# Optimization experiments

Measured on AMD Instinct MI355X. Metric: run time of the kernel, lower is better.

## Reference

```python
import jax, jax.numpy as jnp
from jax import lax
import numpy as np

B, S, D, H, DO, E, K = 4, 2048, 1024, 4096, 1024, 8, 2
CAP_FACTOR = 1.5
LN_EPS = 1e-5


def setup_inputs() -> dict:
    key = jax.random.key(0)
    ks = jax.random.split(key, 8)
    s_in = 1.0 / np.sqrt(D)
    s_h = 1.0 / np.sqrt(H)
    return {
        "x": jax.random.normal(ks[0], (B, S, D), dtype=jnp.float32),
        "router_w": jax.random.normal(ks[1], (D, E), dtype=jnp.float32) * s_in,
        "router_b": jnp.zeros((E,), dtype=jnp.float32),
        "w1": jax.random.normal(ks[2], (E, D, H), dtype=jnp.float32) * s_in,
        "b1": jnp.zeros((E, H), dtype=jnp.float32),
        "w2": jax.random.normal(ks[3], (E, H, DO), dtype=jnp.float32) * s_h,
        "b2": jnp.zeros((E, DO), dtype=jnp.float32),
        "ln_g": jnp.ones((DO,), dtype=jnp.float32),
        "ln_b": jnp.zeros((DO,), dtype=jnp.float32),
    }


def reference(x, router_w, router_b, w1, b1, w2, b2, ln_g, ln_b):
    # Eval-mode (dropout = identity), faithful to SparseDispatcher.forward.
    Bx, Sx, Dx = x.shape
    N = Bx * Sx                               # total tokens
    capacity = max(int(N * CAP_FACTOR / E), K)

    logits = jnp.einsum("bsd,de->bse", x, router_w) + router_b
    probs = jax.nn.softmax(logits, axis=-1)   # [B,S,E]
    topv, topi = lax.top_k(probs, K)          # [B,S,K]
    topv = topv / topv.sum(axis=-1, keepdims=True)

    flat_i = topi.reshape(-1)                 # [N*K] expert ids
    flat_v = topv.reshape(-1)                 # [N*K] combine weights

    # Per-expert capacity selection: keep top-`capacity` assignments by prob.
    mask = flat_i[None, :] == jnp.arange(E)[:, None]          # [E, N*K]
    prio = jnp.where(mask, flat_v[None, :], -1.0)             # [E, N*K]
    pv, pp = lax.top_k(prio, capacity)                        # [E, cap]
    valid = pv > 0.0
    tok = jnp.where(valid, pp // K, 0)                        # token index per slot
    w = jnp.where(valid, pv, 0.0)                             # combine weight (0 if padded)

    x_flat = x.reshape(N, Dx)
    xin = x_flat[tok]                                         # [E, cap, D] gather
    h = jax.nn.gelu(jnp.einsum("ecd,edh->ech", xin, w1) + b1[:, None, :],
                    approximate=False)
    out_e = jnp.einsum("ech,eho->eco", h, w2) + b2[:, None, :]  # [E, cap, DO]
    out_e = out_e * w[..., None]

    out = jnp.zeros((N, DO), dtype=x.dtype)
    out = out.at[tok.reshape(-1)].add(out_e.reshape(-1, DO))  # scatter-combine
    out = out.reshape(Bx, Sx, DO)

    mu = out.mean(axis=-1, keepdims=True)
    var = out.var(axis=-1, keepdims=True)
    out = (out - mu) / jnp.sqrt(var + LN_EPS) * ln_g + ln_b
    return out
```

## Files before the change

### kernel.cpp

```cpp
#include <hip/hip_runtime.h>


typedef unsigned short u16;
typedef unsigned int   u32;
typedef short bf16x8 __attribute__((ext_vector_type(8)));
typedef float f32x4  __attribute__((ext_vector_type(4)));

constexpr int NTOK = 4 * 2048;
constexpr int DIN  = 1024;
constexpr int HID  = 4096;
constexpr int DOUT = 1024;
constexpr int NE   = 8;
constexpr int TOPK = 2;
constexpr int CAP  = 1536;

__device__ __forceinline__ u16 f2bf(float f) {
  u32 u = __float_as_uint(f);
  u32 r = u + 0x7FFFu + ((u >> 16) & 1u);
  return (u16)(r >> 16);
}
__device__ __forceinline__ float bf2f(u16 h) {
  return __uint_as_float(((u32)h) << 16);
}
__device__ __forceinline__ void gload16(const u16* g, u16* l) {
  __builtin_amdgcn_global_load_lds(
      (const __attribute__((address_space(1))) void*)g,
      (__attribute__((address_space(3))) void*)l, 16, 0, 0);
}

__global__ __launch_bounds__(256) void router_topk(
    const float* __restrict__ x, const float* __restrict__ rw,
    const float* __restrict__ rb, int* __restrict__ topi, float* __restrict__ topv)
{
  const int n = blockIdx.x, tid = threadIdx.x, lane = tid & 63, wid = tid >> 6;
  float p[NE] = {0.f,0.f,0.f,0.f,0.f,0.f,0.f,0.f};
  const float* xr = x + (size_t)n * DIN;
  for (int d = tid; d < DIN; d += 256) {
    float xv = xr[d];
    const float* rwd = rw + d * NE;
#pragma unroll
    for (int e = 0; e < NE; e++) p[e] += xv * rwd[e];
  }
#pragma unroll
  for (int e = 0; e < NE; e++)
    for (int o = 32; o; o >>= 1) p[e] += __shfl_down(p[e], o, 64);
  __shared__ float red[4][NE];
  if (lane == 0) {
#pragma unroll
    for (int e = 0; e < NE; e++) red[wid][e] = p[e];
  }
  __syncthreads();
  if (tid == 0) {
    float l[NE], mx = -1e30f;
#pragma unroll
    for (int e = 0; e < NE; e++) {
      l[e] = red[0][e] + red[1][e] + red[2][e] + red[3][e] + rb[e];
      mx = fmaxf(mx, l[e]);
    }
    float s = 0.f, pr[NE];
#pragma unroll
    for (int e = 0; e < NE; e++) { pr[e] = expf(l[e] - mx); s += pr[e]; }
#pragma unroll
    for (int e = 0; e < NE; e++) pr[e] /= s;
    int i0 = 0; float v0 = pr[0];
    for (int e = 1; e < NE; e++) if (pr[e] > v0) { v0 = pr[e]; i0 = e; }
    int i1 = -1; float v1 = -1.f;
    for (int e = 0; e < NE; e++) if (e != i0 && pr[e] > v1) { v1 = pr[e]; i1 = e; }
    float sum = v0 + v1;
    topi[2*n] = i0; topi[2*n+1] = i1;
    topv[2*n] = v0 / sum; topv[2*n+1] = v1 / sum;
  }
}

__global__ void select_caps(const int* __restrict__ topi, const float* __restrict__ topv,
                            u32* __restrict__ t_bits, int* __restrict__ ntie)
{
  const int e = blockIdx.x, tid = threadIdx.x;
  __shared__ u32 hist[256];
  __shared__ u32 s_prefix;
  __shared__ int s_rank, s_done;
  if (tid == 0) { s_prefix = 0u; s_rank = CAP; s_done = 0; }
  __syncthreads();
  for (int byte = 3; byte >= 0; --byte) {
    hist[tid] = 0u;
    __syncthreads();
    const u32 pfx = s_prefix;
    const u32 him = (byte == 3) ? 0u : (0xFFFFFFFFu << ((byte + 1) * 8));
    for (int f = tid; f < NTOK * TOPK; f += 256) {
      if (topi[f] == e) {
        u32 u = __float_as_uint(topv[f]);
        if ((u & him) == pfx) atomicAdd(&hist[(u >> (byte * 8)) & 255u], 1u);
      }
    }
    __syncthreads();
    if (tid == 0) {
      if (byte == 3) {
        int total = 0;
        for (int b = 0; b < 256; b++) total += (int)hist[b];
        if (total <= CAP) { t_bits[e] = 0u; ntie[e] = 0; s_done = 1; }
      }
      if (!s_done) {
        int R = s_rank, cum = 0, b;
        for (b = 255; b >= 0; --b) { cum += (int)hist[b]; if (cum >= R) break; }
        s_prefix = s_prefix | (((u32)b) << (byte * 8));
        s_rank = R - (cum - (int)hist[b]);
      }
    }
    __syncthreads();
    if (s_done) return;
  }
  if (tid == 0) { t_bits[e] = s_prefix; ntie[e] = s_rank; }
}

__global__ __launch_bounds__(256) void assign_slots(
    const int* __restrict__ topi, const float* __restrict__ topv,
    const u32* __restrict__ tb, const int* __restrict__ ntie,
    int* __restrict__ cnt, int* __restrict__ tok,
    float* __restrict__ wsl, int* __restrict__ s_of_t)
{
  const int e = blockIdx.x;
  const int tid = threadIdx.x, lane = tid & 63, wid = tid >> 6;
  const u32 t = tb[e];
  const int nt = ntie[e];
  __shared__ int wtie[4], wkeep[4];
  int run_tie = 0, run_keep = 0;
  const unsigned long long lanemask = (lane == 63) ? ~0ull >> 1 : ((1ull << (lane + 1)) - 1ull) >> 1;
  for (int base = 0; base < NTOK * TOPK; base += 256) {
    const int f = base + tid;
    const bool mine = (topi[f] == e);
    const float v = topv[f];
    const u32 vb = __float_as_uint(v);
    const bool tied  = mine && (vb == t);
    const bool keep0 = mine && (vb > t);
    const unsigned long long mt = __ballot(tied);
    const int tie_pre = __popcll(mt & lanemask);
    if (lane == 0) wtie[wid] = __popcll(mt);
    __syncthreads();
    int tie_base = run_tie;
    for (int w = 0; w < wid; w++) tie_base += wtie[w];
    const bool keep = keep0 || (tied && (tie_base + tie_pre) < nt);
    const unsigned long long mk = __ballot(keep);
    const int keep_pre = __popcll(mk & lanemask);
    if (lane == 0) wkeep[wid] = __popcll(mk);
    __syncthreads();
    int keep_base = run_keep;
    for (int w = 0; w < wid; w++) keep_base += wkeep[w];
    if (mine) {
      int sl = -1;
      if (keep) {
        sl = e * CAP + keep_base + keep_pre;
        tok[sl] = f >> 1;
        wsl[sl] = v;
      }
      s_of_t[f] = sl;
    }
    run_tie  += wtie[0]  + wtie[1]  + wtie[2]  + wtie[3];
    run_keep += wkeep[0] + wkeep[1] + wkeep[2] + wkeep[3];
    __syncthreads();
  }
  if (tid == 0) cnt[e] = run_keep;
}

__global__ __launch_bounds__(256) void gather_x(
    const float* __restrict__ x, const int* __restrict__ tok, const int* __restrict__ cnt,
    u16* __restrict__ Xh, u16* __restrict__ Xl)
{
  const int slot = blockIdx.x;
  const int e = slot / CAP, c = slot % CAP;
  const int tid = threadIdx.x;
  const size_t ob = (size_t)slot * DIN + tid * 4;
  ushort4 h4, l4;
  if (c < cnt[e]) {
    const int n = tok[slot];
    const float4 v = *(const float4*)(x + (size_t)n * DIN + tid * 4);
    u16 h, l;
    h = f2bf(v.x); l = f2bf(v.x - bf2f(h)); h4.x = h; l4.x = l;
    h = f2bf(v.y); l = f2bf(v.y - bf2f(h)); h4.y = h; l4.y = l;
    h = f2bf(v.z); l = f2bf(v.z - bf2f(h)); h4.z = h; l4.z = l;
    h = f2bf(v.w); l = f2bf(v.w - bf2f(h)); h4.w = h; l4.w = l;
  } else {
    h4.x = h4.y = h4.z = h4.w = 0; l4 = h4;
  }
  *(ushort4*)(Xh + ob) = h4;
  *(ushort4*)(Xl + ob) = l4;
}

__global__ __launch_bounds__(256) void transpose_split(
    const float* __restrict__ in, u16* __restrict__ oh, u16* __restrict__ ol,
    int R, int C, int e_off)
{
  const int z = blockIdx.z, e = e_off + z;
  const int c0 = blockIdx.x * 64, r0 = blockIdx.y * 64;
  const int tid = threadIdx.x;
  const int rr = tid >> 4;
  const int cc = (tid & 15) * 4;
  __shared__ float t[64][65];
  const float* ibase = in + (size_t)e * R * C;
#pragma unroll
  for (int q = 0; q < 4; q++) {
    const float4 v = *(const float4*)(ibase + (size_t)(r0 + q * 16 + rr) * C + c0 + cc);
    t[q * 16 + rr][cc + 0] = v.x; t[q * 16 + rr][cc + 1] = v.y;
    t[q * 16 + rr][cc + 2] = v.z; t[q * 16 + rr][cc + 3] = v.w;
  }
  __syncthreads();
  const size_t obase = (size_t)z * C * R;
#pragma unroll
  for (int q = 0; q < 4; q++) {
    const int oc = c0 + q * 16 + rr;
    const int od = r0 + cc;
    ushort4 h4, l4;
    float f; u16 h;
    f = t[cc + 0][q * 16 + rr]; h = f2bf(f); h4.x = h; l4.x = f2bf(f - bf2f(h));
    f = t[cc + 1][q * 16 + rr]; h = f2bf(f); h4.y = h; l4.y = f2bf(f - bf2f(h));
    f = t[cc + 2][q * 16 + rr]; h = f2bf(f); h4.z = h; l4.z = f2bf(f - bf2f(h));
    f = t[cc + 3][q * 16 + rr]; h = f2bf(f); h4.w = h; l4.w = f2bf(f - bf2f(h));
    *(ushort4*)(oh + obase + (size_t)oc * R + od) = h4;
    *(ushort4*)(ol + obase + (size_t)oc * R + od) = l4;
  }
}

template<int NN, int KK, int EPI>
__global__ __launch_bounds__(256, 2) void gemm_mfma(
    const u16* __restrict__ Ah, const u16* __restrict__ Al,
    const u16* __restrict__ Bh, const u16* __restrict__ Bl,
    const float* __restrict__ bias,
    u16* __restrict__ Oh, u16* __restrict__ Ol,
    float* __restrict__ Oe, const float* __restrict__ wslot,
    int e_off)
{
  __shared__ __align__(16) u16 sAh[128 * 32], sAl[128 * 32];
  __shared__ __align__(16) u16 sBh[128 * 32], sBl[128 * 32];
  const int tid = threadIdx.x, lane = tid & 63, wid = tid >> 6;
  const int wm = wid >> 1, wn = wid & 1;
  const int m0 = blockIdx.x * 128, n0 = blockIdx.y * 128, z = blockIdx.z;
  const int eg = e_off + z;

  u16* stile = (wid == 0) ? sAh : (wid == 1) ? sAl : (wid == 2) ? sBh : sBl;
  const u16* gsrc0;
  size_t rowbase;
  if (wid < 2) { gsrc0 = (wid == 0) ? Ah : Al; rowbase = (size_t)z * CAP + m0; }
  else         { gsrc0 = (wid == 2) ? Bh : Bl; rowbase = (size_t)z * NN  + n0; }
  const int srow_l = lane >> 2;
  const int sslot  = lane & 3;

  f32x4 acc[4][4] = {};

  for (int kt = 0; kt < KK; kt += 32) {
    __syncthreads();
#pragma unroll
    for (int i = 0; i < 8; i++) {
      const int row = i * 16 + srow_l;
      const int gslot = sslot ^ ((row >> 2) & 3);
      const u16* src = gsrc0 + (rowbase + row) * (size_t)KK + (kt + gslot * 8);
      gload16(src, stile + i * 512);
    }
    __syncthreads();

    bf16x8 afh[4], afl[4], bfh[4], bfl[4];
#pragma unroll
    for (int mf = 0; mf < 4; mf++) {
      const int r = wm * 64 + mf * 16 + (lane & 15);
      const int off = r * 32 + (((lane >> 4) ^ ((r >> 2) & 3)) * 8);
      afh[mf] = *(const bf16x8*)(sAh + off);
      afl[mf] = *(const bf16x8*)(sAl + off);
    }
#pragma unroll
    for (int nf = 0; nf < 4; nf++) {
      const int r = wn * 64 + nf * 16 + (lane & 15);
      const int off = r * 32 + (((lane >> 4) ^ ((r >> 2) & 3)) * 8);
      bfh[nf] = *(const bf16x8*)(sBh + off);
      bfl[nf] = *(const bf16x8*)(sBl + off);
    }
#pragma unroll
    for (int mf = 0; mf < 4; mf++) {
#pragma unroll
      for (int nf = 0; nf < 4; nf++) {
        acc[mf][nf] = __builtin_amdgcn_mfma_f32_16x16x32_bf16(afh[mf], bfh[nf], acc[mf][nf], 0, 0, 0);
        acc[mf][nf] = __builtin_amdgcn_mfma_f32_16x16x32_bf16(afh[mf], bfl[nf], acc[mf][nf], 0, 0, 0);
        acc[mf][nf] = __builtin_amdgcn_mfma_f32_16x16x32_bf16(afl[mf], bfh[nf], acc[mf][nf], 0, 0, 0);
      }
    }
  }

#pragma unroll
  for (int mf = 0; mf < 4; mf++) {
#pragma unroll
    for (int nf = 0; nf < 4; nf++) {
      const int col = n0 + wn * 64 + nf * 16 + (lane & 15);
      const float bv = bias[(size_t)eg * NN + col];
#pragma unroll
      for (int r = 0; r < 4; r++) {
        const int row = m0 + wm * 64 + mf * 16 + (lane >> 4) * 4 + r;
        const float v = acc[mf][nf][r] + bv;
        if constexpr (EPI == 0) {
          const float gel = 0.5f * v * (1.0f + erff(v * 0.70710678118654752f));
          const u16 hh = f2bf(gel);
          const u16 ll = f2bf(gel - bf2f(hh));
          const size_t o = ((size_t)z * CAP + row) * NN + col;
          Oh[o] = hh; Ol[o] = ll;
        } else {
          const int slot = eg * CAP + row;
          Oe[(size_t)slot * DOUT + col] = v * wslot[slot];
        }
      }
    }
  }
}

__global__ __launch_bounds__(256) void combine_ln(
    const float* __restrict__ oute, const int* __restrict__ s_of_t,
    const float* __restrict__ gam, const float* __restrict__ bet,
    float* __restrict__ out)
{
  const int n = blockIdx.x, tid = threadIdx.x, lane = tid & 63, wid = tid >> 6;
  __shared__ float sred[4];
  const int s0 = s_of_t[2 * n], s1 = s_of_t[2 * n + 1];
  const int idx = tid * 4;
  float y0 = 0.f, y1 = 0.f, y2 = 0.f, y3 = 0.f;
  if (s0 >= 0) {
    const float4 a = *(const float4*)(oute + (size_t)s0 * DOUT + idx);
    y0 = a.x; y1 = a.y; y2 = a.z; y3 = a.w;
  }
  if (s1 >= 0) {
    const float4 a = *(const float4*)(oute + (size_t)s1 * DOUT + idx);
    y0 += a.x; y1 += a.y; y2 += a.z; y3 += a.w;
  }
  float ssum = y0 + y1 + y2 + y3;
  for (int o = 32; o; o >>= 1) ssum += __shfl_down(ssum, o, 64);
  if (lane == 0) sred[wid] = ssum;
  __syncthreads();
  const float mu = (sred[0] + sred[1] + sred[2] + sred[3]) * (1.f / DOUT);
  __syncthreads();
  const float d0 = y0 - mu, d1 = y1 - mu, d2 = y2 - mu, d3 = y3 - mu;
  float sq = d0 * d0 + d1 * d1 + d2 * d2 + d3 * d3;
  for (int o = 32; o; o >>= 1) sq += __shfl_down(sq, o, 64);
  if (lane == 0) sred[wid] = sq;
  __syncthreads();
  const float var = (sred[0] + sred[1] + sred[2] + sred[3]) * (1.f / DOUT);
  const float inv = 1.0f / sqrtf(var + 1e-5f);
  float4 o4;
  o4.x = d0 * inv * gam[idx + 0] + bet[idx + 0];
  o4.y = d1 * inv * gam[idx + 1] + bet[idx + 1];
  o4.z = d2 * inv * gam[idx + 2] + bet[idx + 2];
  o4.w = d3 * inv * gam[idx + 3] + bet[idx + 3];
  *(float4*)(out + (size_t)n * DOUT + idx) = o4;
}

extern "C" void kernel_launch(void* const* d_in, const int* in_sizes, int n_in,
                              void* d_out, int out_size, void* d_ws, size_t ws_size,
                              hipStream_t stream)
{
  const float* x   = (const float*)d_in[0];
  const float* rw  = (const float*)d_in[1];
  const float* rb  = (const float*)d_in[2];
  const float* w1  = (const float*)d_in[3];
  const float* b1  = (const float*)d_in[4];
  const float* w2  = (const float*)d_in[5];
  const float* b2  = (const float*)d_in[6];
  const float* lng = (const float*)d_in[7];
  const float* lnb = (const float*)d_in[8];
  float* out = (float*)d_out;

  char* base = (char*)d_ws;
  size_t off = 0;
  auto alloc = [&](size_t bytes) -> void* {
    void* p = base + off;
    off = (off + bytes + 255) & ~(size_t)255;
    return p;
  };
  int*   topi = (int*)  alloc((size_t)NTOK * TOPK * 4);
  float* topv = (float*)alloc((size_t)NTOK * TOPK * 4);
  u32*   tb   = (u32*)  alloc(NE * 4);
  int*   ntie = (int*)  alloc(NE * 4);
  int*   cnt  = (int*)  alloc(NE * 4);
  int*   tok  = (int*)  alloc((size_t)NE * CAP * 4);
  float* wsl  = (float*)alloc((size_t)NE * CAP * 4);
  int*   soft = (int*)  alloc((size_t)NTOK * TOPK * 4);
  u16*   Xh   = (u16*)  alloc((size_t)NE * CAP * DIN * 2);
  u16*   Xl   = (u16*)  alloc((size_t)NE * CAP * DIN * 2);
  float* oute = (float*)alloc((size_t)NE * CAP * DOUT * 4);
  const size_t fixed = off;

  const size_t perE = 2 * ((size_t)DIN * HID * 2) + 2 * ((size_t)HID * DOUT * 2)
                    + 2 * ((size_t)CAP * HID * 2);
  int G = 1;
  for (int g = 8; g >= 1; g >>= 1) {
    if (fixed + (size_t)g * perE + 8192 <= ws_size) { G = g; break; }
  }
  u16* W1Th = (u16*)alloc((size_t)G * DIN * HID * 2);
  u16* W1Tl = (u16*)alloc((size_t)G * DIN * HID * 2);
  u16* W2Th = (u16*)alloc((size_t)G * HID * DOUT * 2);
  u16* W2Tl = (u16*)alloc((size_t)G * HID * DOUT * 2);
  u16* hh   = (u16*)alloc((size_t)G * CAP * HID * 2);
  u16* hl   = (u16*)alloc((size_t)G * CAP * HID * 2);

  router_topk<<<NTOK, 256, 0, stream>>>(x, rw, rb, topi, topv);
  select_caps<<<NE, 256, 0, stream>>>(topi, topv, tb, ntie);
  assign_slots<<<NE, 256, 0, stream>>>(topi, topv, tb, ntie, cnt, tok, wsl, soft);
  gather_x<<<NE * CAP, 256, 0, stream>>>(x, tok, cnt, Xh, Xl);

  for (int g0 = 0; g0 < NE; g0 += G) {
    transpose_split<<<dim3(HID / 64, DIN / 64, G), 256, 0, stream>>>(w1, W1Th, W1Tl, DIN, HID, g0);
    transpose_split<<<dim3(DOUT / 64, HID / 64, G), 256, 0, stream>>>(w2, W2Th, W2Tl, HID, DOUT, g0);
    gemm_mfma<HID, DIN, 0><<<dim3(CAP / 128, HID / 128, G), 256, 0, stream>>>(
        Xh + (size_t)g0 * CAP * DIN, Xl + (size_t)g0 * CAP * DIN,
        W1Th, W1Tl, b1, hh, hl, nullptr, nullptr, g0);
    gemm_mfma<DOUT, HID, 1><<<dim3(CAP / 128, DOUT / 128, G), 256, 0, stream>>>(
        hh, hl, W2Th, W2Tl, b2, nullptr, nullptr, oute, wsl, g0);
  }

  combine_ln<<<NTOK, 256, 0, stream>>>(oute, soft, lng, lnb, out);
}
```

Measured before the change: 1.350 ms.

## Double-buffer GEMM loads, split-K the second GEMM, remap blocks across XCDs

The MFMA GEMM kernel now double-buffers shared-memory tiles, issuing loads two k-steps ahead with explicit vmcnt waits and raised wave priority around the MFMAs. Workgroup IDs are remapped so neighbouring tiles land on the same XCD for better L2 reuse. The second GEMM is split four ways along K and accumulates into a zeroed output with atomicAdd, raising parallelism. The GELU epilogue is staged through shared memory so stores are vectorised. The costs are doubled LDS use, which may reduce occupancy, atomic traffic, an extra memset, and nondeterministic summation order.

```diff
diff --git a/kernel.cpp b/kernel.cpp
--- a/kernel.cpp
+++ b/kernel.cpp
@@ -219,7 +219,7 @@
   }
 }
 
-template<int NN, int KK, int EPI>
+template<int NN, int FULLK, int CHUNKK, int EPI, int KSPLIT>
 __global__ __launch_bounds__(256, 2) void gemm_mfma(
     const u16* __restrict__ Ah, const u16* __restrict__ Al,
     const u16* __restrict__ Bh, const u16* __restrict__ Bl,
@@ -228,49 +228,78 @@
     float* __restrict__ Oe, const float* __restrict__ wslot,
     int e_off)
 {
-  __shared__ __align__(16) u16 sAh[128 * 32], sAl[128 * 32];
-  __shared__ __align__(16) u16 sBh[128 * 32], sBl[128 * 32];
+  constexpr int NT = CHUNKK / 32;
+  constexpr int SMEM = (EPI == 0) ? (4 * 64 * 65 * 4) : 65536;
+  __shared__ __align__(16) char smem[SMEM];
+  u16* st = (u16*)smem;
+
   const int tid = threadIdx.x, lane = tid & 63, wid = tid >> 6;
   const int wm = wid >> 1, wn = wid & 1;
-  const int m0 = blockIdx.x * 128, n0 = blockIdx.y * 128, z = blockIdx.z;
-  const int eg = e_off + z;
-
-  u16* stile = (wid == 0) ? sAh : (wid == 1) ? sAl : (wid == 2) ? sBh : sBl;
-  const u16* gsrc0;
-  size_t rowbase;
-  if (wid < 2) { gsrc0 = (wid == 0) ? Ah : Al; rowbase = (size_t)z * CAP + m0; }
-  else         { gsrc0 = (wid == 2) ? Bh : Bl; rowbase = (size_t)z * NN  + n0; }
-  const int srow_l = lane >> 2;
-  const int sslot  = lane & 3;
+
+  const int gx = gridDim.x, gy = gridDim.y;
+  const int nwg = gx * gy * gridDim.z;
+  int wg = blockIdx.x + gx * (blockIdx.y + gy * blockIdx.z);
+  {
+    const int xcd = wg & 7, rest = wg >> 3;
+    const int q = nwg >> 3, r = nwg & 7;
+    wg = (xcd < r ? xcd * (q + 1) : r * (q + 1) + (xcd - r) * q) + rest;
+  }
+  const int bx = wg % gx; int t2 = wg / gx;
+  const int by = t2 % gy; const int bzz = t2 / gy;
+  const int zi = bzz / KSPLIT, kc = bzz % KSPLIT;
+  const int m0 = bx * 128, n0 = by * 128;
+  const int eg = e_off + zi;
+  const size_t kbase = (size_t)kc * CHUNKK;
+
+  const size_t a0 = ((size_t)zi * CAP + m0) * FULLK + kbase;
+  const size_t b0 = ((size_t)zi * NN  + n0) * FULLK + kbase;
+  const u16* gsrc[4] = {Ah + a0, Al + a0, Bh + b0, Bl + b0};
+
+  auto STAGE = [&](int cb, int kt) {
+#pragma unroll
+    for (int i = 0; i < 8; i++) {
+      const int s   = i * 256 + tid;
+      const int p   = s >> 9;
+      const int q   = s & 511;
+      const int row = q >> 2;
+      const int gsl = (q & 3) ^ ((row >> 2) & 3);
+      const u16* src = gsrc[p] + (size_t)row * FULLK + kt * 32 + gsl * 8;
+      const int q0  = (i * 256 + (tid & 192)) & 511;
+      u16* dst = st + (((cb << 2) + p) << 12) + q0 * 8;
+      gload16(src, dst);
+    }
+  };
 
   f32x4 acc[4][4] = {};
 
-  for (int kt = 0; kt < KK; kt += 32) {
-    __syncthreads();
-#pragma unroll
-    for (int i = 0; i < 8; i++) {
-      const int row = i * 16 + srow_l;
-      const int gslot = sslot ^ ((row >> 2) & 3);
-      const u16* src = gsrc0 + (rowbase + row) * (size_t)KK + (kt + gslot * 8);
-      gload16(src, stile + i * 512);
-    }
-    __syncthreads();
-
+  STAGE(0, 0);
+  STAGE(1, 1);
+  int cur = 0;
+  for (int kt = 0; kt < NT; ++kt) {
+    if (kt != NT - 1) { asm volatile("s_waitcnt vmcnt(8)" ::: "memory"); }
+    else             { asm volatile("s_waitcnt vmcnt(0)" ::: "memory"); }
+    __builtin_amdgcn_s_barrier();
+
+    const u16* pAh = st + (((cur << 2) + 0) << 12);
+    const u16* pAl = st + (((cur << 2) + 1) << 12);
+    const u16* pBh = st + (((cur << 2) + 2) << 12);
+    const u16* pBl = st + (((cur << 2) + 3) << 12);
     bf16x8 afh[4], afl[4], bfh[4], bfl[4];
 #pragma unroll
     for (int mf = 0; mf < 4; mf++) {
       const int r = wm * 64 + mf * 16 + (lane & 15);
-      const int off = r * 32 + (((lane >> 4) ^ ((r >> 2) & 3)) * 8);
-      afh[mf] = *(const bf16x8*)(sAh + off);
-      afl[mf] = *(const bf16x8*)(sAl + off);
+      const int off = r * 32 + (((lane >> 4) ^ ((r >> 2) & 3)) << 3);
+      afh[mf] = *(const bf16x8*)(pAh + off);
+      afl[mf] = *(const bf16x8*)(pAl + off);
     }
 #pragma unroll
     for (int nf = 0; nf < 4; nf++) {
       const int r = wn * 64 + nf * 16 + (lane & 15);
-      const int off = r * 32 + (((lane >> 4) ^ ((r >> 2) & 3)) * 8);
-      bfh[nf] = *(const bf16x8*)(sBh + off);
-      bfl[nf] = *(const bf16x8*)(sBl + off);
-    }
+      const int off = r * 32 + (((lane >> 4) ^ ((r >> 2) & 3)) << 3);
+      bfh[nf] = *(const bf16x8*)(pBh + off);
+      bfl[nf] = *(const bf16x8*)(pBl + off);
+    }
+    __builtin_amdgcn_s_setprio(1);
 #pragma unroll
     for (int mf = 0; mf < 4; mf++) {
 #pragma unroll
@@ -280,27 +309,56 @@
         acc[mf][nf] = __builtin_amdgcn_mfma_f32_16x16x32_bf16(afl[mf], bfh[nf], acc[mf][nf], 0, 0, 0);
       }
     }
-  }
-
-#pragma unroll
-  for (int mf = 0; mf < 4; mf++) {
-#pragma unroll
-    for (int nf = 0; nf < 4; nf++) {
-      const int col = n0 + wn * 64 + nf * 16 + (lane & 15);
-      const float bv = bias[(size_t)eg * NN + col];
-#pragma unroll
-      for (int r = 0; r < 4; r++) {
-        const int row = m0 + wm * 64 + mf * 16 + (lane >> 4) * 4 + r;
-        const float v = acc[mf][nf][r] + bv;
-        if constexpr (EPI == 0) {
-          const float gel = 0.5f * v * (1.0f + erff(v * 0.70710678118654752f));
-          const u16 hh = f2bf(gel);
-          const u16 ll = f2bf(gel - bf2f(hh));
-          const size_t o = ((size_t)z * CAP + row) * NN + col;
-          Oh[o] = hh; Ol[o] = ll;
-        } else {
+    __builtin_amdgcn_s_setprio(0);
+    __builtin_amdgcn_sched_barrier(0);
+    __builtin_amdgcn_s_barrier();
+    __builtin_amdgcn_sched_barrier(0);
+    if (kt + 2 < NT) STAGE(cur, kt + 2);
+    cur ^= 1;
+  }
+
+  if constexpr (EPI == 0) {
+    float* epi = (float*)smem + wid * (64 * 65);
+#pragma unroll
+    for (int mf = 0; mf < 4; mf++)
+#pragma unroll
+      for (int nf = 0; nf < 4; nf++)
+#pragma unroll
+        for (int r = 0; r < 4; r++)
+          epi[(mf * 16 + (lane >> 4) * 4 + r) * 65 + nf * 16 + (lane & 15)] = acc[mf][nf][r];
+    const float* brow = bias + (size_t)eg * NN + n0 + wn * 64;
+#pragma unroll
+    for (int it = 0; it < 16; ++it) {
+      const int rr = it * 4 + (lane >> 4);
+      const int cc = (lane & 15) * 4;
+      float4 v = *(const float4*)&epi[rr * 65 + cc];
+      const float4 bv = *(const float4*)(brow + cc);
+      ushort4 h4, l4; u16 h; float g;
+      g = v.x + bv.x; g = 0.5f * g * (1.0f + erff(g * 0.70710678118654752f));
+      h = f2bf(g); h4.x = h; l4.x = f2bf(g - bf2f(h));
+      g = v.y + bv.y; g = 0.5f * g * (1.0f + erff(g * 0.70710678118654752f));
+      h = f2bf(g); h4.y = h; l4.y = f2bf(g - bf2f(h));
+      g = v.z + bv.z; g = 0.5f * g * (1.0f + erff(g * 0.70710678118654752f));
+      h = f2bf(g); h4.z = h; l4.z = f2bf(g - bf2f(h));
+      g = v.w + bv.w; g = 0.5f * g * (1.0f + erff(g * 0.70710678118654752f));
+      h = f2bf(g); h4.w = h; l4.w = f2bf(g - bf2f(h));
+      const size_t o = ((size_t)zi * CAP + m0 + wm * 64 + rr) * NN + n0 + wn * 64 + cc;
+      *(ushort4*)(Oh + o) = h4;
+      *(ushort4*)(Ol + o) = l4;
+    }
+  } else {
+#pragma unroll
+    for (int mf = 0; mf < 4; mf++) {
+#pragma unroll
+      for (int nf = 0; nf < 4; nf++) {
+        const int col = n0 + wn * 64 + nf * 16 + (lane & 15);
+        const float bv = (kc == 0) ? bias[(size_t)eg * NN + col] : 0.0f;
+#pragma unroll
+        for (int r = 0; r < 4; r++) {
+          const int row = m0 + wm * 64 + mf * 16 + (lane >> 4) * 4 + r;
           const int slot = eg * CAP + row;
-          Oe[(size_t)slot * DOUT + col] = v * wslot[slot];
+          const float contrib = (acc[mf][nf][r] + bv) * wslot[slot];
+          atomicAdd(&Oe[(size_t)slot * NN + col], contrib);
         }
       }
     }
@@ -398,14 +456,15 @@
   select_caps<<<NE, 256, 0, stream>>>(topi, topv, tb, ntie);
   assign_slots<<<NE, 256, 0, stream>>>(topi, topv, tb, ntie, cnt, tok, wsl, soft);
   gather_x<<<NE * CAP, 256, 0, stream>>>(x, tok, cnt, Xh, Xl);
+  hipMemsetAsync(oute, 0, (size_t)NE * CAP * DOUT * 4, stream);
 
   for (int g0 = 0; g0 < NE; g0 += G) {
     transpose_split<<<dim3(HID / 64, DIN / 64, G), 256, 0, stream>>>(w1, W1Th, W1Tl, DIN, HID, g0);
     transpose_split<<<dim3(DOUT / 64, HID / 64, G), 256, 0, stream>>>(w2, W2Th, W2Tl, HID, DOUT, g0);
-    gemm_mfma<HID, DIN, 0><<<dim3(CAP / 128, HID / 128, G), 256, 0, stream>>>(
+    gemm_mfma<HID, DIN, DIN, 0, 1><<<dim3(CAP / 128, HID / 128, G), 256, 0, stream>>>(
         Xh + (size_t)g0 * CAP * DIN, Xl + (size_t)g0 * CAP * DIN,
         W1Th, W1Tl, b1, hh, hl, nullptr, nullptr, g0);
-    gemm_mfma<DOUT, HID, 1><<<dim3(CAP / 128, DOUT / 128, G), 256, 0, stream>>>(
+    gemm_mfma<DOUT, HID, 1024, 1, 4><<<dim3(CAP / 128, DOUT / 128, G * 4), 256, 0, stream>>>(
         hh, hl, W2Th, W2Tl, b2, nullptr, nullptr, oute, wsl, g0);
   }
 
```

Result: faster. 1.263 ms (-6.4%).
